# Kernel optimization log

Hardware: AMD Instinct MI355X
Metric: run time of the kernel (lower is better)

Reference implementation:

```python
import jax, jax.numpy as jnp
import numpy as np

TRUST_W, SIM_W, STALE_W = 0.4, 0.4, 0.2
EPS = 1e-8  # torch cosine_similarity norm clamp


def setup_inputs() -> dict:
    key = jax.random.key(0)
    ks = jax.random.split(key, 6)
    B, D, E, C = 8192, 1024, 32, 256
    x = jax.random.normal(ks[0], (B, D), dtype=jnp.float32)
    expert_features = jax.random.normal(ks[1], (E, D), dtype=jnp.float32)
    trust = jax.random.uniform(ks[2], (E,), dtype=jnp.float32)
    staleness = jax.random.uniform(ks[3], (E,), dtype=jnp.float32)
    W = jax.random.normal(ks[4], (E, C, D), dtype=jnp.float32) * 0.02
    b = jax.random.normal(ks[5], (E, C), dtype=jnp.float32) * 0.02
    return {"x": x, "expert_features": expert_features, "trust": trust,
            "staleness": staleness, "W": W, "b": b, "k": 4}


def reference(x, expert_features, trust, staleness, W, b, k):
    # --- scoring: trust + cosine similarity + staleness, per (token, expert) ---
    xn = x / jnp.maximum(jnp.linalg.norm(x, axis=-1, keepdims=True), EPS)
    efn = expert_features / jnp.maximum(
        jnp.linalg.norm(expert_features, axis=-1, keepdims=True), EPS)
    cos = xn @ efn.T                              # [B, E]
    sim = (cos + 1.0) * 0.5
    stale_score = jnp.maximum(0.0, 1.0 - staleness)  # [E]
    scores = TRUST_W * trust + SIM_W * sim + STALE_W * stale_score  # [B, E]

    # --- top-k expert selection per token ---
    _, idx = jax.lax.top_k(scores, k)             # [B, k] int32

    # --- grouped expert heads: dense all-expert GEMM, then gather top-k ---
    all_out = jnp.einsum('bd,ecd->bec', x, W) + b  # [B, E, C]
    sel = jnp.take_along_axis(all_out, idx[:, :, None], axis=1)  # [B, k, C]
    return sel.mean(axis=1)                        # [B, C]
```

## Files before the change

kernel.cpp:

```cpp
#include <hip/hip_runtime.h>
#include <math.h>

#define KMAX 8
#define CSTRIDE 64

typedef short s16x8 __attribute__((ext_vector_type(8)));
typedef float f32x4 __attribute__((ext_vector_type(4)));

__device__ inline ushort f2bf(float f) {
    union { float f; unsigned u; } v; v.f = f;
    unsigned r = v.u + 0x7fffu + ((v.u >> 16) & 1u);
    return (ushort)(r >> 16);
}
__device__ inline float bf2f(ushort b) {
    union { unsigned u; float f; } v; v.u = ((unsigned)b) << 16; return v.f;
}

__device__ inline void gload_lds16(const void* g, void* l) {
    __builtin_amdgcn_global_load_lds(
        (const __attribute__((address_space(1))) unsigned int*)g,
        (__attribute__((address_space(3))) unsigned int*)l, 16, 0, 0);
}

__global__ void k_efnorm(const float* __restrict__ ef, int D,
                         double* __restrict__ efn, int* __restrict__ counts) {
    int e = blockIdx.x;
    int lane = threadIdx.x;
    if (lane == 0) counts[e * CSTRIDE] = 0;
    double s = 0.0;
    for (int i = lane; i < D; i += 64) {
        double v = (double)ef[(size_t)e * D + i];
        s = fma(v, v, s);
    }
    #pragma unroll
    for (int off = 32; off > 0; off >>= 1) s += __shfl_xor(s, off);
    if (lane == 0) efn[e] = sqrt(s);
}

__global__ __launch_bounds__(256) void k_prep_w(
    const float* __restrict__ W, const int* __restrict__ counts,
    int perExpF4, ushort* __restrict__ wbf, int* __restrict__ offs) {
    int e = blockIdx.y;
    if (blockIdx.x == 0 && e == 0 && threadIdx.x == 0) {
        int s = 0;
        for (int e2 = 0; e2 < 32; ++e2) { offs[e2] = s; s += counts[e2 * CSTRIDE]; }
    }
    if (counts[e * CSTRIDE] == 0) return;
    size_t base = (size_t)e * perExpF4;
    #pragma unroll
    for (int j = 0; j < 4; ++j) {
        int idx = (blockIdx.x * 4 + j) * 256 + threadIdx.x;
        if (idx < perExpF4) {
            float4 v = *(const float4*)&W[(base + idx) * 4];
            ushort4 u;
            u.x = f2bf(v.x); u.y = f2bf(v.y); u.z = f2bf(v.z); u.w = f2bf(v.w);
            *(ushort4*)&wbf[(base + idx) * 4] = u;
        }
    }
}

__global__ __launch_bounds__(256) void k_scores3(
    const float* __restrict__ x, const float* __restrict__ ef,
    const float* __restrict__ trust, const float* __restrict__ stale,
    const double* __restrict__ efn, const int* __restrict__ kp,
    int D, int B, ushort* __restrict__ xbf,
    int* __restrict__ counts, int* __restrict__ lists, int* __restrict__ sel)
{
    __shared__ float xs[16 * 64];
    __shared__ float efs[32 * 64];
    __shared__ double sc[16 * 33];
    __shared__ int bcnt[32];
    __shared__ int bbase[32];
    __shared__ unsigned char selb[16 * KMAX];
    __shared__ unsigned char lposb[16 * KMAX];

    int tid = threadIdx.x;
    int tp = tid >> 4, eg = tid & 15;
    int tb = blockIdx.x * 16;

    if (tid < 32) bcnt[tid] = 0;

    int rx = tid >> 4, qx = tid & 15;
    int re0 = tid >> 4, re1 = 16 + (tid >> 4);
    int qe = tid & 15;

    int nch = D / 64;

    float4 vx  = *(const float4*)&x[(size_t)(tb + rx) * D + qx * 4];
    float4 ve0 = *(const float4*)&ef[(size_t)re0 * D + qe * 4];
    float4 ve1 = *(const float4*)&ef[(size_t)re1 * D + qe * 4];

    double acc0 = 0.0, acc1 = 0.0, axx = 0.0;

    for (int ch = 0; ch < nch; ++ch) {
        *(float4*)&xs[rx * 64 + ((qx ^ rx) << 2)] = vx;
        {
            ushort4 u;
            u.x = f2bf(vx.x); u.y = f2bf(vx.y); u.z = f2bf(vx.z); u.w = f2bf(vx.w);
            *(ushort4*)&xbf[(size_t)(tb + rx) * D + ch * 64 + qx * 4] = u;
        }
        *(float4*)&efs[re0 * 64 + ((qe ^ (re0 & 15)) << 2)] = ve0;
        *(float4*)&efs[re1 * 64 + ((qe ^ (re1 & 15)) << 2)] = ve1;
        __syncthreads();

        if (ch + 1 < nch) {
            int k1 = (ch + 1) * 64;
            vx  = *(const float4*)&x[(size_t)(tb + rx) * D + k1 + qx * 4];
            ve0 = *(const float4*)&ef[(size_t)re0 * D + k1 + qe * 4];
            ve1 = *(const float4*)&ef[(size_t)re1 * D + k1 + qe * 4];
        }

        float a0 = 0.f, a1 = 0.f, ax = 0.f;
        #pragma unroll
        for (int q = 0; q < 16; ++q) {
            float4 xv = *(const float4*)&xs[tp * 64 + ((q ^ tp) << 2)];
            float4 e0 = *(const float4*)&efs[eg * 64 + ((q ^ eg) << 2)];
            float4 e1 = *(const float4*)&efs[(eg + 16) * 64 + ((q ^ eg) << 2)];
            a0 = fmaf(xv.x, e0.x, a0); a0 = fmaf(xv.y, e0.y, a0);
            a0 = fmaf(xv.z, e0.z, a0); a0 = fmaf(xv.w, e0.w, a0);
            a1 = fmaf(xv.x, e1.x, a1); a1 = fmaf(xv.y, e1.y, a1);
            a1 = fmaf(xv.z, e1.z, a1); a1 = fmaf(xv.w, e1.w, a1);
            ax = fmaf(xv.x, xv.x, ax); ax = fmaf(xv.y, xv.y, ax);
            ax = fmaf(xv.z, xv.z, ax); ax = fmaf(xv.w, xv.w, ax);
        }
        __syncthreads();
        acc0 += (double)a0; acc1 += (double)a1; axx += (double)ax;
    }

    double xn = fmax(sqrt(axx), 1e-8);
    {
        int e0i = eg;
        double en0 = fmax(efn[e0i], 1e-8);
        sc[tp * 33 + e0i] = 0.4 * (double)trust[e0i]
            + 0.2 * (acc0 / (xn * en0) + 1.0)
            + 0.2 * fmax(0.0, 1.0 - (double)stale[e0i]);
        int e1i = eg + 16;
        double en1 = fmax(efn[e1i], 1e-8);
        sc[tp * 33 + e1i] = 0.4 * (double)trust[e1i]
            + 0.2 * (acc1 / (xn * en1) + 1.0)
            + 0.2 * fmax(0.0, 1.0 - (double)stale[e1i]);
    }
    __syncthreads();

    int kk = kp[0]; kk = kk < 1 ? 1 : (kk > KMAX ? KMAX : kk);

    if (tid < 16) {
        unsigned mask = 0;
        for (int p = 0; p < kk; ++p) {
            double bv = -1e300; int be = 0;
            #pragma unroll
            for (int e = 0; e < 32; ++e) {
                double v = sc[tid * 33 + e];
                if (!((mask >> e) & 1u) && v > bv) { bv = v; be = e; }
            }
            mask |= 1u << be;
            selb[tid * KMAX + p] = (unsigned char)be;
            lposb[tid * KMAX + p] = (unsigned char)atomicAdd(&bcnt[be], 1);
        }
    }
    __syncthreads();
    if (tid < 32) {
        int c = bcnt[tid];
        bbase[tid] = c ? atomicAdd(&counts[tid * CSTRIDE], c) : 0;
    }
    __syncthreads();
    if (tid < 16) {
        int t = tb + tid;
        for (int p = 0; p < kk; ++p) {
            int e = selb[tid * KMAX + p];
            int pos = bbase[e] + lposb[tid * KMAX + p];
            lists[(size_t)e * B + pos] = t;
            sel[(size_t)t * KMAX + p] = (e << 24) | pos;
        }
    }
}

__global__ __launch_bounds__(512) void k_moe3(
    const ushort* __restrict__ xbf, const ushort* __restrict__ wbf,
    const float* __restrict__ bias, const int* __restrict__ lists,
    const int* __restrict__ counts, const int* __restrict__ offs,
    const int* __restrict__ kp, int B, int C, int D,
    int usePart, ushort* __restrict__ part, float* __restrict__ out)
{
    int e = blockIdx.z;
    int cnt = counts[e * CSTRIDE];
    int row0 = blockIdx.x * 128;
    if (row0 >= cnt) return;
    int col0 = blockIdx.y * 128;
    int nt = min(128, cnt - row0);

    __shared__ ushort xs[128 * 64];
    __shared__ ushort wsh[128 * 64];
    __shared__ int toks[128];

    int tid = threadIdx.x;
    if (tid < 128) toks[tid] = (tid < nt) ? lists[(size_t)e * B + row0 + tid] : 0;
    __syncthreads();

    int lane = tid & 63, wid = tid >> 6;
    int wr = wid >> 1, wc = wid & 1;
    int l15 = lane & 15, l16 = lane >> 4;

    f32x4 acc[2][4];
    #pragma unroll
    for (int m = 0; m < 2; ++m)
        #pragma unroll
        for (int n = 0; n < 4; ++n) acc[m][n] = (f32x4){0.f, 0.f, 0.f, 0.f};

    int nch = D / 64;
    for (int ch = 0; ch < nch; ++ch) {
        int k0 = ch * 64;
        #pragma unroll
        for (int t = 0; t < 2; ++t) {
            int id = t * 512 + tid;
            int r = id >> 3, seg = id & 7;
            int ssw = (seg ^ (r & 7)) << 3;
            gload_lds16(&xbf[(size_t)toks[r] * D + k0 + ssw],
                        (char*)xs + (size_t)(t * 512 + wid * 64) * 16);
        }
        #pragma unroll
        for (int t = 0; t < 2; ++t) {
            int id = t * 512 + tid;
            int r = id >> 3, seg = id & 7;
            int ssw = (seg ^ (r & 7)) << 3;
            gload_lds16(&wbf[((size_t)e * C + col0 + r) * D + k0 + ssw],
                        (char*)wsh + (size_t)(t * 512 + wid * 64) * 16);
        }
        __syncthreads();
        #pragma unroll
        for (int ks = 0; ks < 2; ++ks) {
            s16x8 a[2], bfr[4];
            int sbase = ks * 4 + l16;
            #pragma unroll
            for (int m = 0; m < 2; ++m) {
                int r = wr * 32 + m * 16 + l15;
                a[m] = *(const s16x8*)&xs[r * 64 + ((sbase ^ (l15 & 7)) << 3)];
            }
            #pragma unroll
            for (int n = 0; n < 4; ++n) {
                int r = wc * 64 + n * 16 + l15;
                bfr[n] = *(const s16x8*)&wsh[r * 64 + ((sbase ^ (l15 & 7)) << 3)];
            }
            #pragma unroll
            for (int m = 0; m < 2; ++m)
                #pragma unroll
                for (int n = 0; n < 4; ++n)
                    acc[m][n] = __builtin_amdgcn_mfma_f32_16x16x32_bf16(
                        a[m], bfr[n], acc[m][n], 0, 0, 0);
        }
        __syncthreads();
    }

    int kk = kp[0]; kk = kk < 1 ? 1 : (kk > KMAX ? KMAX : kk);
    if (usePart) {
        int slotBase = offs[e] + row0;
        #pragma unroll
        for (int m = 0; m < 2; ++m) {
            int rbase = wr * 32 + m * 16 + l16 * 4;
            #pragma unroll
            for (int n = 0; n < 4; ++n) {
                int col = col0 + wc * 64 + n * 16 + l15;
                float bv = bias[(size_t)e * C + col];
                #pragma unroll
                for (int r = 0; r < 4; ++r) {
                    int rl = rbase + r;
                    if (rl < nt)
                        part[(size_t)(slotBase + rl) * C + col] =
                            f2bf(acc[m][n][r] + bv);
                }
            }
        }
    } else {
        float invk = 1.0f / (float)kk;
        #pragma unroll
        for (int m = 0; m < 2; ++m) {
            int rbase = wr * 32 + m * 16 + l16 * 4;
            #pragma unroll
            for (int n = 0; n < 4; ++n) {
                int col = col0 + wc * 64 + n * 16 + l15;
                float bv = bias[(size_t)e * C + col];
                #pragma unroll
                for (int r = 0; r < 4; ++r) {
                    int rl = rbase + r;
                    if (rl < nt)
                        atomicAdd(&out[(size_t)toks[rl] * C + col],
                                  invk * (acc[m][n][r] + bv));
                }
            }
        }
    }
}

__global__ __launch_bounds__(256) void k_combine(
    const ushort* __restrict__ part, const int* __restrict__ sel,
    const int* __restrict__ offs, const int* __restrict__ kp,
    int C, float* __restrict__ out)
{
    int kk = kp[0]; kk = kk < 1 ? 1 : (kk > KMAX ? KMAX : kk);
    float invk = 1.0f / (float)kk;
    int sub = threadIdx.x >> 6, lane = threadIdx.x & 63;
    int t = blockIdx.x * 4 + sub;
    for (int c = lane * 4; c < C; c += 256) {
        float s0 = 0.f, s1 = 0.f, s2 = 0.f, s3 = 0.f;
        for (int p = 0; p < kk; ++p) {
            int sv = sel[(size_t)t * KMAX + p];
            int slot = offs[sv >> 24] + (sv & 0xFFFFFF);
            ushort4 u = *(const ushort4*)&part[(size_t)slot * C + c];
            s0 += bf2f(u.x); s1 += bf2f(u.y); s2 += bf2f(u.z); s3 += bf2f(u.w);
        }
        float4 o = make_float4(invk * s0, invk * s1, invk * s2, invk * s3);
        *(float4*)&out[(size_t)t * C + c] = o;
    }
}

__global__ __launch_bounds__(256) void k_scores_legacy(
    const float* __restrict__ x, const float* __restrict__ ef,
    const float* __restrict__ trust, const float* __restrict__ stale,
    const double* __restrict__ efn, const int* __restrict__ kp,
    int D, int B, int* __restrict__ counts, int* __restrict__ lists)
{
    __shared__ float xs[32][72];
    __shared__ float efs[32][72];
    __shared__ double sc[32][33];

    int tid = threadIdx.x;
    int tl = tid >> 3, eg = tid & 7;
    int tb = blockIdx.x * 32;

    double acc[4] = {0, 0, 0, 0};
    double axx = 0.0;
    int nch = D / 64;

    for (int ch = 0; ch < nch; ++ch) {
        #pragma unroll
        for (int t = 0; t < 2; ++t) {
            int id = t * 256 + tid;
            int r = id >> 4, q = id & 15;
            float4 v = *(const float4*)&x[(size_t)(tb + r) * D + ch * 64 + q * 4];
            *(float4*)&xs[r][q * 4] = v;
            float4 w = *(const float4*)&ef[(size_t)r * D + ch * 64 + q * 4];
            *(float4*)&efs[r][q * 4] = w;
        }
        __syncthreads();
        #pragma unroll 4
        for (int q = 0; q < 16; ++q) {
            float4 xv = *(const float4*)&xs[tl][q * 4];
            double x0 = xv.x, x1 = xv.y, x2 = xv.z, x3 = xv.w;
            axx = fma(x0, x0, fma(x1, x1, fma(x2, x2, fma(x3, x3, axx))));
            #pragma unroll
            for (int j = 0; j < 4; ++j) {
                float4 ev = *(const float4*)&efs[eg + 8 * j][q * 4];
                acc[j] = fma(x0, (double)ev.x, acc[j]);
                acc[j] = fma(x1, (double)ev.y, acc[j]);
                acc[j] = fma(x2, (double)ev.z, acc[j]);
                acc[j] = fma(x3, (double)ev.w, acc[j]);
            }
        }
        __syncthreads();
    }

    double xn = fmax(sqrt(axx), 1e-8);
    #pragma unroll
    for (int j = 0; j < 4; ++j) {
        int e = eg + 8 * j;
        double en = fmax(efn[e], 1e-8);
        double cosv = acc[j] / (xn * en);
        sc[tl][e] = 0.4 * (double)trust[e] + 0.2 * (cosv + 1.0)
                  + 0.2 * fmax(0.0, 1.0 - (double)stale[e]);
    }
    __syncthreads();

    if (tid < 32) {
        int kk = kp[0]; kk = kk < 1 ? 1 : (kk > KMAX ? KMAX : kk);
        unsigned mask = 0;
        int t = tb + tid;
        for (int p = 0; p < kk; ++p) {
            double bv = -1e300; int be = 0;
            #pragma unroll
            for (int e = 0; e < 32; ++e) {
                double v = sc[tid][e];
                if (!((mask >> e) & 1u) && v > bv) { bv = v; be = e; }
            }
            mask |= 1u << be;
            int pos = atomicAdd(&counts[be * CSTRIDE], 1);
            lists[(size_t)be * B + pos] = t;
        }
    }
}

__global__ __launch_bounds__(512) void k_moe_f32(
    const float* __restrict__ x, const float* __restrict__ W,
    const float* __restrict__ bias, const int* __restrict__ lists,
    const int* __restrict__ counts, const int* __restrict__ kp,
    int B, int C, int D, float* __restrict__ out)
{
    int e = blockIdx.z;
    int cnt = counts[e * CSTRIDE];
    int row0 = blockIdx.x * 128;
    if (row0 >= cnt) return;
    int col0 = blockIdx.y * 256;
    int nt = min(128, cnt - row0);

    __shared__ ushort xs[128 * 72];
    __shared__ ushort wsh[256 * 72];
    __shared__ int toks[128];

    int tid = threadIdx.x;
    if (tid < 128) toks[tid] = (tid < nt) ? lists[(size_t)e * B + row0 + tid] : 0;
    __syncthreads();

    int lane = tid & 63, wid = tid >> 6;
    int wr = wid >> 2, wc = wid & 3;
    int l15 = lane & 15, l16 = lane >> 4;

    f32x4 acc[4][4];
    #pragma unroll
    for (int m = 0; m < 4; ++m)
        #pragma unroll
        for (int n = 0; n < 4; ++n) acc[m][n] = (f32x4){0.f, 0.f, 0.f, 0.f};

    int nch = D / 64;
    for (int ch = 0; ch < nch; ++ch) {
        int k0 = ch * 64;
        #pragma unroll
        for (int t = 0; t < 4; ++t) {
            int id = t * 512 + tid;
            int r = id >> 4, q = id & 15;
            float4 v = (r < nt)
                ? *(const float4*)&x[(size_t)toks[r] * D + k0 + q * 4]
                : make_float4(0.f, 0.f, 0.f, 0.f);
            ushort4 u;
            u.x = f2bf(v.x); u.y = f2bf(v.y); u.z = f2bf(v.z); u.w = f2bf(v.w);
            *(ushort4*)&xs[r * 72 + q * 4] = u;
        }
        #pragma unroll
        for (int t = 0; t < 8; ++t) {
            int id = t * 512 + tid;
            int r = id >> 4, q = id & 15;
            float4 v = *(const float4*)&W[((size_t)e * C + col0 + r) * D + k0 + q * 4];
            ushort4 u;
            u.x = f2bf(v.x); u.y = f2bf(v.y); u.z = f2bf(v.z); u.w = f2bf(v.w);
            *(ushort4*)&wsh[r * 72 + q * 4] = u;
        }
        __syncthreads();
        #pragma unroll
        for (int ks = 0; ks < 2; ++ks) {
            s16x8 a[4], bfr[4];
            #pragma unroll
            for (int m = 0; m < 4; ++m)
                a[m] = *(const s16x8*)&xs[(wr * 64 + m * 16 + l15) * 72 + ks * 32 + l16 * 8];
            #pragma unroll
            for (int n = 0; n < 4; ++n)
                bfr[n] = *(const s16x8*)&wsh[(wc * 64 + n * 16 + l15) * 72 + ks * 32 + l16 * 8];
            #pragma unroll
            for (int m = 0; m < 4; ++m)
                #pragma unroll
                for (int n = 0; n < 4; ++n)
                    acc[m][n] = __builtin_amdgcn_mfma_f32_16x16x32_bf16(
                        a[m], bfr[n], acc[m][n], 0, 0, 0);
        }
        __syncthreads();
    }

    int kk = kp[0]; kk = kk < 1 ? 1 : (kk > KMAX ? KMAX : kk);
    float invk = 1.0f / (float)kk;
    #pragma unroll
    for (int m = 0; m < 4; ++m) {
        int rbase = wr * 64 + m * 16 + l16 * 4;
        #pragma unroll
        for (int n = 0; n < 4; ++n) {
            int col = col0 + wc * 64 + n * 16 + l15;
            float bv = bias[(size_t)e * C + col];
            #pragma unroll
            for (int r = 0; r < 4; ++r) {
                int rl = rbase + r;
                if (rl < nt)
                    atomicAdd(&out[(size_t)toks[rl] * C + col],
                              invk * (acc[m][n][r] + bv));
            }
        }
    }
}

extern "C" void kernel_launch(void* const* d_in, const int* in_sizes, int n_in,
                              void* d_out, int out_size, void* d_ws, size_t ws_size,
                              hipStream_t stream) {
    const float* x     = (const float*)d_in[0];
    const float* ef    = (const float*)d_in[1];
    const float* trust = (const float*)d_in[2];
    const float* stale = (const float*)d_in[3];
    const float* W     = (const float*)d_in[4];
    const float* b     = (const float*)d_in[5];
    const int*   kp    = (const int*)d_in[6];

    int E = in_sizes[2];
    int D = in_sizes[1] / E;
    int B = in_sizes[0] / D;
    int C = in_sizes[5] / E;
    float* out = (float*)d_out;

    char* ws = (char*)d_ws;
    double* efn   = (double*)ws;
    int*    counts= (int*)(ws + 256);
    size_t off_offs = 256 + 32 * CSTRIDE * 4;
    int*    offs  = (int*)(ws + off_offs);
    size_t off_sel = off_offs + 256;
    int*    sel   = (int*)(ws + off_sel);
    size_t off_lists = off_sel + (size_t)B * KMAX * 4;
    int*    lists = (int*)(ws + off_lists);
    size_t off_xbf = off_lists + (size_t)E * B * 4;
    off_xbf = (off_xbf + 255) & ~(size_t)255;
    ushort* xbf = (ushort*)(ws + off_xbf);
    size_t off_wbf = off_xbf + (size_t)B * D * 2;
    ushort* wbf = (ushort*)(ws + off_wbf);
    size_t off_part = off_wbf + (size_t)E * C * D * 2;
    off_part = (off_part + 255) & ~(size_t)255;
    ushort* part = (ushort*)(ws + off_part);
    size_t need_mid  = off_part;
    size_t need_full = off_part + (size_t)B * KMAX * C * 2;

    bool fullPath = ws_size >= need_mid;
    int usePart = (fullPath && ws_size >= need_full) ? 1 : 0;

    if (!usePart)
        hipMemsetAsync(d_out, 0, (size_t)out_size * sizeof(float), stream);

    k_efnorm<<<E, 64, 0, stream>>>(ef, D, efn, counts);

    if (fullPath) {
        k_scores3<<<B / 16, 256, 0, stream>>>(x, ef, trust, stale, efn,
                                              kp, D, B, xbf, counts, lists, sel);
        int perExpF4 = (C * D) / 4;
        dim3 wgrid((perExpF4 + 1023) / 1024, E);
        k_prep_w<<<wgrid, 256, 0, stream>>>(W, counts, perExpF4, wbf, offs);
        dim3 grid((B + 127) / 128, C / 128, E);
        k_moe3<<<grid, 512, 0, stream>>>(xbf, wbf, b, lists, counts, offs, kp,
                                         B, C, D, usePart, part, out);
        if (usePart)
            k_combine<<<B / 4, 256, 0, stream>>>(part, sel, offs, kp, C, out);
    } else {
        k_scores_legacy<<<B / 32, 256, 0, stream>>>(x, ef, trust, stale, efn,
                                                    kp, D, B, counts, lists);
        dim3 grid((B + 127) / 128, C / 256, E);
        k_moe_f32<<<grid, 512, 0, stream>>>(x, W, b, lists, counts, kp,
                                            B, C, D, out);
    }
}
```

Measured before the change: 83.84 us.

## Split scoring kernel along D into two partial-dot blocks plus a top-k kernel

The scoring kernel is split in two. The first kernel launches twice as many blocks, each reducing half of the D dimension, and writes partial dot products and partial squared norms as doubles to workspace. The second kernel sums the two halves, computes the scores, runs top-k for 128 tokens per block, and builds the expert lists. The goal is more parallelism and a shorter serial K loop in the scoring pass, at the cost of an extra launch, global round-trips for the partials, and a top-k stage that now runs with fewer blocks.

```diff
diff --git a/kernel.cpp b/kernel.cpp
--- a/kernel.cpp
+++ b/kernel.cpp
@@ -59,52 +59,45 @@
     }
 }
 
-__global__ __launch_bounds__(256) void k_scores3(
+__global__ __launch_bounds__(256) void k_scores3a(
     const float* __restrict__ x, const float* __restrict__ ef,
-    const float* __restrict__ trust, const float* __restrict__ stale,
-    const double* __restrict__ efn, const int* __restrict__ kp,
     int D, int B, ushort* __restrict__ xbf,
-    int* __restrict__ counts, int* __restrict__ lists, int* __restrict__ sel)
+    double* __restrict__ pacc, double* __restrict__ paxx)
 {
     __shared__ float xs[16 * 64];
     __shared__ float efs[32 * 64];
-    __shared__ double sc[16 * 33];
-    __shared__ int bcnt[32];
-    __shared__ int bbase[32];
-    __shared__ unsigned char selb[16 * KMAX];
-    __shared__ unsigned char lposb[16 * KMAX];
 
     int tid = threadIdx.x;
     int tp = tid >> 4, eg = tid & 15;
-    int tb = blockIdx.x * 16;
-
-    if (tid < 32) bcnt[tid] = 0;
+    int g = blockIdx.x >> 1, h = blockIdx.x & 1;
+    int tb = g * 16;
+    int kbase = h * (D >> 1);
+    int nch = D >> 7;
 
     int rx = tid >> 4, qx = tid & 15;
     int re0 = tid >> 4, re1 = 16 + (tid >> 4);
     int qe = tid & 15;
 
-    int nch = D / 64;
-
-    float4 vx  = *(const float4*)&x[(size_t)(tb + rx) * D + qx * 4];
-    float4 ve0 = *(const float4*)&ef[(size_t)re0 * D + qe * 4];
-    float4 ve1 = *(const float4*)&ef[(size_t)re1 * D + qe * 4];
+    float4 vx  = *(const float4*)&x[(size_t)(tb + rx) * D + kbase + qx * 4];
+    float4 ve0 = *(const float4*)&ef[(size_t)re0 * D + kbase + qe * 4];
+    float4 ve1 = *(const float4*)&ef[(size_t)re1 * D + kbase + qe * 4];
 
     double acc0 = 0.0, acc1 = 0.0, axx = 0.0;
 
     for (int ch = 0; ch < nch; ++ch) {
+        int k0 = kbase + ch * 64;
         *(float4*)&xs[rx * 64 + ((qx ^ rx) << 2)] = vx;
         {
             ushort4 u;
             u.x = f2bf(vx.x); u.y = f2bf(vx.y); u.z = f2bf(vx.z); u.w = f2bf(vx.w);
-            *(ushort4*)&xbf[(size_t)(tb + rx) * D + ch * 64 + qx * 4] = u;
+            *(ushort4*)&xbf[(size_t)(tb + rx) * D + k0 + qx * 4] = u;
         }
         *(float4*)&efs[re0 * 64 + ((qe ^ (re0 & 15)) << 2)] = ve0;
         *(float4*)&efs[re1 * 64 + ((qe ^ (re1 & 15)) << 2)] = ve1;
         __syncthreads();
 
         if (ch + 1 < nch) {
-            int k1 = (ch + 1) * 64;
+            int k1 = kbase + (ch + 1) * 64;
             vx  = *(const float4*)&x[(size_t)(tb + rx) * D + k1 + qx * 4];
             ve0 = *(const float4*)&ef[(size_t)re0 * D + k1 + qe * 4];
             ve1 = *(const float4*)&ef[(size_t)re1 * D + k1 + qe * 4];
@@ -127,24 +120,47 @@
         acc0 += (double)a0; acc1 += (double)a1; axx += (double)ax;
     }
 
+    int tt = tb + tp;
+    pacc[(size_t)(h * 32 + eg) * B + tt] = acc0;
+    pacc[(size_t)(h * 32 + eg + 16) * B + tt] = acc1;
+    if (eg == 0) paxx[(size_t)h * B + tt] = axx;
+}
+
+__global__ __launch_bounds__(256) void k_scores3b(
+    const float* __restrict__ trust, const float* __restrict__ stale,
+    const double* __restrict__ efn, const double* __restrict__ pacc,
+    const double* __restrict__ paxx, const int* __restrict__ kp,
+    int B, int* __restrict__ counts, int* __restrict__ lists,
+    int* __restrict__ sel)
+{
+    __shared__ double sc[128 * 33];
+    __shared__ int bcnt[32];
+    __shared__ int bbase[32];
+    __shared__ unsigned char selb[128 * KMAX];
+    __shared__ unsigned char lposb[128 * KMAX];
+
+    int tid = threadIdx.x;
+    int tk = tid & 127, eh = tid >> 7;
+    int t = blockIdx.x * 128 + tk;
+
+    if (tid < 32) bcnt[tid] = 0;
+
+    double axx = paxx[t] + paxx[(size_t)B + t];
     double xn = fmax(sqrt(axx), 1e-8);
-    {
-        int e0i = eg;
-        double en0 = fmax(efn[e0i], 1e-8);
-        sc[tp * 33 + e0i] = 0.4 * (double)trust[e0i]
-            + 0.2 * (acc0 / (xn * en0) + 1.0)
-            + 0.2 * fmax(0.0, 1.0 - (double)stale[e0i]);
-        int e1i = eg + 16;
-        double en1 = fmax(efn[e1i], 1e-8);
-        sc[tp * 33 + e1i] = 0.4 * (double)trust[e1i]
-            + 0.2 * (acc1 / (xn * en1) + 1.0)
-            + 0.2 * fmax(0.0, 1.0 - (double)stale[e1i]);
+    #pragma unroll
+    for (int j = 0; j < 16; ++j) {
+        int e = eh * 16 + j;
+        double dot = pacc[(size_t)e * B + t] + pacc[(size_t)(32 + e) * B + t];
+        double en = fmax(efn[e], 1e-8);
+        sc[tk * 33 + e] = 0.4 * (double)trust[e]
+            + 0.2 * (dot / (xn * en) + 1.0)
+            + 0.2 * fmax(0.0, 1.0 - (double)stale[e]);
     }
     __syncthreads();
 
     int kk = kp[0]; kk = kk < 1 ? 1 : (kk > KMAX ? KMAX : kk);
 
-    if (tid < 16) {
+    if (tid < 128) {
         unsigned mask = 0;
         for (int p = 0; p < kk; ++p) {
             double bv = -1e300; int be = 0;
@@ -164,13 +180,13 @@
         bbase[tid] = c ? atomicAdd(&counts[tid * CSTRIDE], c) : 0;
     }
     __syncthreads();
-    if (tid < 16) {
-        int t = tb + tid;
+    if (tid < 128) {
+        int tt = blockIdx.x * 128 + tid;
         for (int p = 0; p < kk; ++p) {
             int e = selb[tid * KMAX + p];
             int pos = bbase[e] + lposb[tid * KMAX + p];
-            lists[(size_t)e * B + pos] = t;
-            sel[(size_t)t * KMAX + p] = (e << 24) | pos;
+            lists[(size_t)e * B + pos] = tt;
+            sel[(size_t)tt * KMAX + p] = (e << 24) | pos;
         }
     }
 }
@@ -508,7 +524,12 @@
     int*    sel   = (int*)(ws + off_sel);
     size_t off_lists = off_sel + (size_t)B * KMAX * 4;
     int*    lists = (int*)(ws + off_lists);
-    size_t off_xbf = off_lists + (size_t)E * B * 4;
+    size_t off_pacc = off_lists + (size_t)E * B * 4;
+    off_pacc = (off_pacc + 255) & ~(size_t)255;
+    double* pacc  = (double*)(ws + off_pacc);
+    size_t off_paxx = off_pacc + (size_t)64 * B * 8;
+    double* paxx  = (double*)(ws + off_paxx);
+    size_t off_xbf = off_paxx + (size_t)2 * B * 8;
     off_xbf = (off_xbf + 255) & ~(size_t)255;
     ushort* xbf = (ushort*)(ws + off_xbf);
     size_t off_wbf = off_xbf + (size_t)B * D * 2;
@@ -528,8 +549,10 @@
     k_efnorm<<<E, 64, 0, stream>>>(ef, D, efn, counts);
 
     if (fullPath) {
-        k_scores3<<<B / 16, 256, 0, stream>>>(x, ef, trust, stale, efn,
-                                              kp, D, B, xbf, counts, lists, sel);
+        k_scores3a<<<(B / 16) * 2, 256, 0, stream>>>(x, ef, D, B, xbf,
+                                                     pacc, paxx);
+        k_scores3b<<<B / 128, 256, 0, stream>>>(trust, stale, efn, pacc, paxx,
+                                                kp, B, counts, lists, sel);
         int perExpF4 = (C * D) / 4;
         dim3 wgrid((perExpF4 + 1023) / 1024, E);
         k_prep_w<<<wgrid, 256, 0, stream>>>(W, counts, perExpF4, wbf, offs);
```

After: 81.97 us. -2.2%, faster.
